# Performance work log

Hardware: AMD Instinct MI355X
Metric: run time of the kernel (lower is better)

The kernel has to match this reference:

```python
import jax, jax.numpy as jnp
import numpy as np

INPUT_CHANNELS = 64
OUT_CHANNELS = 64
OUT_DIM = 4
IN_FEAT = INPUT_CHANNELS * OUT_DIM * 2   # 512
OUT_FEAT = OUT_CHANNELS * OUT_DIM        # 256
BATCH = 65536


def setup_inputs() -> dict:
    key = jax.random.key(0)
    k_x, k_w, k_b = jax.random.split(key, 3)
    x = jax.random.normal(k_x, (BATCH, IN_FEAT), dtype=jnp.float32)
    weight = jax.random.normal(k_w, (OUT_FEAT, IN_FEAT), dtype=jnp.float32)
    bias = jax.random.normal(k_b, (1, OUT_FEAT), dtype=jnp.float32)
    return {"x": x, "weight": weight, "bias": bias}


def reference(x, weight, bias) -> jnp.ndarray:
    # Original: (x[:, None] * weight).sum(-1) / sqrt(input_channels) + 0.1*bias
    # Mathematically identical to a GEMM: x @ weight.T
    scale = 1.0 / jnp.sqrt(jnp.asarray(INPUT_CHANNELS, dtype=x.dtype))
    out = jnp.einsum('bi,oi->bo', x, weight) * scale  # [B, out_feat]
    out = out + bias * 0.1
    return out
```

## Files before the change

### kernel.cpp

```cpp
#include <hip/hip_runtime.h>
#include <hip/hip_bf16.h>


typedef __bf16 bf16;
typedef __attribute__((ext_vector_type(8))) __bf16 bf16x8;
typedef __attribute__((ext_vector_type(4))) __bf16 bf16x4;
typedef __attribute__((ext_vector_type(4))) float f32x4;

#define BATCH_ 65536
#define KDIM   512
#define NDIM   256
#define ROWS_PER_CHUNK   32
#define CHUNKS_PER_BLOCK 8
#define ROWS_PER_BLOCK   256
#define BN_BLOCK 128
#define BN_WAVE  16

__global__ __launch_bounds__(256) void wcvt_kernel(const float* __restrict__ w,
                                                   bf16* __restrict__ wb) {
    int i = (blockIdx.x * 256 + threadIdx.x) * 4;
    f32x4 v = *(const f32x4*)(w + i);
    bf16x4 o;
    o[0] = (bf16)(v.x * 0.125f);
    o[1] = (bf16)(v.y * 0.125f);
    o[2] = (bf16)(v.z * 0.125f);
    o[3] = (bf16)(v.w * 0.125f);
    *(bf16x4*)(wb + i) = o;
}

__global__ __launch_bounds__(512, 2) void gemm_kernel(const float* __restrict__ x,
                                                      const bf16* __restrict__ wb,
                                                      const float* __restrict__ bias,
                                                      float* __restrict__ out) {
    __shared__ __align__(16) char lds[2][32 * 1024];

    const int tid  = threadIdx.x;
    const int lane = tid & 63;
    const int w    = tid >> 6;
    const int q    = lane >> 4;
    const int l16  = lane & 15;

    const int  ng = blockIdx.x & 1;
    const long mg = blockIdx.x >> 1;
    const long row_base = mg * ROWS_PER_BLOCK;
    const int  n0 = ng * BN_BLOCK + w * BN_WAVE;

    bf16x8 wf[16];
#pragma unroll
    for (int kc = 0; kc < 16; ++kc)
        wf[kc] = *(const bf16x8*)(wb + (long)(n0 + l16) * KDIM + kc * 32 + q * 8);

    const float bv = 0.1f * bias[n0 + l16];

    const float* xw = x + (row_base + (long)w * 4) * KDIM + lane * 4;

    f32x4 ld[8];
#pragma unroll
    for (int j = 0; j < 4; ++j)
#pragma unroll
        for (int h = 0; h < 2; ++h)
            ld[j * 2 + h] = *(const f32x4*)(xw + (long)j * KDIM + h * 256);

    for (int t = 0; t < CHUNKS_PER_BLOCK; ++t) {
        char* buf = lds[t & 1];

#pragma unroll
        for (int j = 0; j < 4; ++j) {
            const int rr = w * 4 + j;
#pragma unroll
            for (int h = 0; h < 2; ++h) {
                f32x4 v = ld[j * 2 + h];
                bf16x4 o;
                o[0] = (bf16)v.x; o[1] = (bf16)v.y;
                o[2] = (bf16)v.z; o[3] = (bf16)v.w;
                const int g  = h * 32 + (lane >> 1);
                const int gs = g ^ (rr & 7);
                *(bf16x4*)(buf + rr * 1024 + gs * 16 + (lane & 1) * 8) = o;
            }
        }

        __syncthreads();

        if (t + 1 < CHUNKS_PER_BLOCK) {
#pragma unroll
            for (int j = 0; j < 4; ++j)
#pragma unroll
                for (int h = 0; h < 2; ++h)
                    ld[j * 2 + h] = *(const f32x4*)(xw + ((long)(t + 1) * 32 + j) * KDIM + h * 256);
        }

        f32x4 acc[2];
        acc[0] = (f32x4)0.0f;
        acc[1] = (f32x4)0.0f;
#pragma unroll
        for (int kc = 0; kc < 16; ++kc) {
#pragma unroll
            for (int mt = 0; mt < 2; ++mt) {
                const int rr = mt * 16 + l16;
                const int gs = (kc * 4 + q) ^ (rr & 7);
                bf16x8 a = *(const bf16x8*)(buf + rr * 1024 + gs * 16);
                acc[mt] = __builtin_amdgcn_mfma_f32_16x16x32_bf16(a, wf[kc], acc[mt], 0, 0, 0);
            }
        }

        const long row0 = row_base + (long)t * ROWS_PER_CHUNK;
#pragma unroll
        for (int mt = 0; mt < 2; ++mt)
#pragma unroll
            for (int r = 0; r < 4; ++r)
                out[(row0 + mt * 16 + q * 4 + r) * NDIM + n0 + l16] = acc[mt][r] + bv;
    }
}

extern "C" void kernel_launch(void* const* d_in, const int* in_sizes, int n_in,
                              void* d_out, int out_size, void* d_ws, size_t ws_size,
                              hipStream_t stream) {
    const float* x    = (const float*)d_in[0];
    const float* w    = (const float*)d_in[1];
    const float* bias = (const float*)d_in[2];
    float* out = (float*)d_out;
    bf16* wb   = (bf16*)d_ws;

    wcvt_kernel<<<(NDIM * KDIM) / (256 * 4), 256, 0, stream>>>(w, wb);
    gemm_kernel<<<(BATCH_ / ROWS_PER_BLOCK) * (NDIM / BN_BLOCK), 512, 0, stream>>>(x, wb, bias, out);
}
```

Before: 233.9 us.

## Compute full N per block and stage fp32 x directly into LDS

Each block now computes all 256 output columns instead of half, so every x row is read from global memory once rather than twice. x chunks are copied straight into LDS as fp32 using global_load_lds with double buffering, and the bf16 conversion moves to the LDS read just before the MFMA. The trade-offs are that each wave now keeps twice as many weight fragments in registers, which risks spills under the 512x2 launch bound. The unswizzled fp32 row-major LDS layout may also cause bank conflicts.

After: 230.9 us. No clear change (-1.3%).

```diff
diff --git a/kernel.cpp b/kernel.cpp
--- a/kernel.cpp
+++ b/kernel.cpp
@@ -10,11 +10,10 @@
 #define BATCH_ 65536
 #define KDIM   512
 #define NDIM   256
-#define ROWS_PER_CHUNK   32
-#define CHUNKS_PER_BLOCK 8
-#define ROWS_PER_BLOCK   256
-#define BN_BLOCK 128
-#define BN_WAVE  16
+#define CHUNK_ROWS 16
+#define CHUNKS 16
+#define ROWS_PER_BLOCK (CHUNK_ROWS * CHUNKS)
+#define CHUNK_BYTES (CHUNK_ROWS * KDIM * 4)
 
 __global__ __launch_bounds__(256) void wcvt_kernel(const float* __restrict__ w,
                                                    bf16* __restrict__ wb) {
@@ -28,87 +27,99 @@
     *(bf16x4*)(wb + i) = o;
 }
 
+__device__ __forceinline__ void stage_chunk(const float* xc, float* buf, int tid) {
+#pragma unroll
+    for (int p = 0; p < 4; ++p) {
+        const char* g = (const char*)xc + p * 8192 + tid * 16;
+        char* l = (char*)buf + p * 8192 + (tid >> 6) * 1024;
+        __builtin_amdgcn_global_load_lds(
+            (const __attribute__((address_space(1))) void*)g,
+            (__attribute__((address_space(3))) void*)l, 16, 0, 0);
+    }
+}
+
+__device__ __forceinline__ bf16x8 cvt_a(f32x4 lo, f32x4 hi) {
+    bf16x8 a;
+    a[0] = (bf16)lo.x; a[1] = (bf16)lo.y; a[2] = (bf16)lo.z; a[3] = (bf16)lo.w;
+    a[4] = (bf16)hi.x; a[5] = (bf16)hi.y; a[6] = (bf16)hi.z; a[7] = (bf16)hi.w;
+    return a;
+}
+
+__device__ __forceinline__ void compute_chunk(const float* buf,
+                                              const bf16x8 (&wf)[16][2],
+                                              int l16, int q, f32x4 (&acc)[2]) {
+    acc[0] = (f32x4)0.0f;
+    acc[1] = (f32x4)0.0f;
+    const float* rowp = buf + l16 * KDIM + q * 8;
+#pragma unroll
+    for (int kc = 0; kc < 16; ++kc) {
+        f32x4 lo = *(const f32x4*)(rowp + kc * 32);
+        f32x4 hi = *(const f32x4*)(rowp + kc * 32 + 4);
+        bf16x8 a = cvt_a(lo, hi);
+        acc[0] = __builtin_amdgcn_mfma_f32_16x16x32_bf16(a, wf[kc][0], acc[0], 0, 0, 0);
+        acc[1] = __builtin_amdgcn_mfma_f32_16x16x32_bf16(a, wf[kc][1], acc[1], 0, 0, 0);
+    }
+}
+
 __global__ __launch_bounds__(512, 2) void gemm_kernel(const float* __restrict__ x,
                                                       const bf16* __restrict__ wb,
                                                       const float* __restrict__ bias,
                                                       float* __restrict__ out) {
-    __shared__ __align__(16) char lds[2][32 * 1024];
+    __shared__ __align__(16) float bufA[CHUNK_ROWS * KDIM];
+    __shared__ __align__(16) float bufB[CHUNK_ROWS * KDIM];
 
     const int tid  = threadIdx.x;
     const int lane = tid & 63;
     const int w    = tid >> 6;
     const int q    = lane >> 4;
     const int l16  = lane & 15;
+    const int n0   = w * 32;
+    const long row_base = (long)blockIdx.x * ROWS_PER_BLOCK;
 
-    const int  ng = blockIdx.x & 1;
-    const long mg = blockIdx.x >> 1;
-    const long row_base = mg * ROWS_PER_BLOCK;
-    const int  n0 = ng * BN_BLOCK + w * BN_WAVE;
-
-    bf16x8 wf[16];
+    bf16x8 wf[16][2];
 #pragma unroll
     for (int kc = 0; kc < 16; ++kc)
-        wf[kc] = *(const bf16x8*)(wb + (long)(n0 + l16) * KDIM + kc * 32 + q * 8);
+#pragma unroll
+        for (int nt = 0; nt < 2; ++nt)
+            wf[kc][nt] = *(const bf16x8*)(wb + (long)(n0 + nt * 16 + l16) * KDIM
+                                             + kc * 32 + q * 8);
+    float bv[2];
+    bv[0] = 0.1f * bias[n0 + l16];
+    bv[1] = 0.1f * bias[n0 + 16 + l16];
 
-    const float bv = 0.1f * bias[n0 + l16];
+    const float* xblk = x + row_base * KDIM;
 
-    const float* xw = x + (row_base + (long)w * 4) * KDIM + lane * 4;
+    stage_chunk(xblk, bufA, tid);
+    __syncthreads();
 
-    f32x4 ld[8];
+    f32x4 acc[2];
+#pragma unroll 1
+    for (int t = 0; t < CHUNKS; t += 2) {
+        if (t + 1 < CHUNKS)
+            stage_chunk(xblk + (long)(t + 1) * CHUNK_ROWS * KDIM, bufB, tid);
+        compute_chunk(bufA, wf, l16, q, acc);
+        __syncthreads();
+        {
+            const long row0 = row_base + (long)t * CHUNK_ROWS;
 #pragma unroll
-    for (int j = 0; j < 4; ++j)
+            for (int nt = 0; nt < 2; ++nt)
 #pragma unroll
-        for (int h = 0; h < 2; ++h)
-            ld[j * 2 + h] = *(const f32x4*)(xw + (long)j * KDIM + h * 256);
-
-    for (int t = 0; t < CHUNKS_PER_BLOCK; ++t) {
-        char* buf = lds[t & 1];
-
-#pragma unroll
-        for (int j = 0; j < 4; ++j) {
-            const int rr = w * 4 + j;
-#pragma unroll
-            for (int h = 0; h < 2; ++h) {
-                f32x4 v = ld[j * 2 + h];
-                bf16x4 o;
-                o[0] = (bf16)v.x; o[1] = (bf16)v.y;
-                o[2] = (bf16)v.z; o[3] = (bf16)v.w;
-                const int g  = h * 32 + (lane >> 1);
-                const int gs = g ^ (rr & 7);
-                *(bf16x4*)(buf + rr * 1024 + gs * 16 + (lane & 1) * 8) = o;
-            }
+                for (int r = 0; r < 4; ++r)
+                    out[(row0 + q * 4 + r) * NDIM + n0 + nt * 16 + l16] = acc[nt][r] + bv[nt];
         }
 
+        if (t + 2 < CHUNKS)
+            stage_chunk(xblk + (long)(t + 2) * CHUNK_ROWS * KDIM, bufA, tid);
+        compute_chunk(bufB, wf, l16, q, acc);
         __syncthreads();
-
-        if (t + 1 < CHUNKS_PER_BLOCK) {
+        {
+            const long row0 = row_base + (long)(t + 1) * CHUNK_ROWS;
 #pragma unroll
-            for (int j = 0; j < 4; ++j)
+            for (int nt = 0; nt < 2; ++nt)
 #pragma unroll
-                for (int h = 0; h < 2; ++h)
-                    ld[j * 2 + h] = *(const f32x4*)(xw + ((long)(t + 1) * 32 + j) * KDIM + h * 256);
+                for (int r = 0; r < 4; ++r)
+                    out[(row0 + q * 4 + r) * NDIM + n0 + nt * 16 + l16] = acc[nt][r] + bv[nt];
         }
-
-        f32x4 acc[2];
-        acc[0] = (f32x4)0.0f;
-        acc[1] = (f32x4)0.0f;
-#pragma unroll
-        for (int kc = 0; kc < 16; ++kc) {
-#pragma unroll
-            for (int mt = 0; mt < 2; ++mt) {
-                const int rr = mt * 16 + l16;
-                const int gs = (kc * 4 + q) ^ (rr & 7);
-                bf16x8 a = *(const bf16x8*)(buf + rr * 1024 + gs * 16);
-                acc[mt] = __builtin_amdgcn_mfma_f32_16x16x32_bf16(a, wf[kc], acc[mt], 0, 0, 0);
-            }
-        }
-
-        const long row0 = row_base + (long)t * ROWS_PER_CHUNK;
-#pragma unroll
-        for (int mt = 0; mt < 2; ++mt)
-#pragma unroll
-            for (int r = 0; r < 4; ++r)
-                out[(row0 + mt * 16 + q * 4 + r) * NDIM + n0 + l16] = acc[mt][r] + bv;
     }
 }
 
@@ -122,5 +133,5 @@
     bf16* wb   = (bf16*)d_ws;
 
     wcvt_kernel<<<(NDIM * KDIM) / (256 * 4), 256, 0, stream>>>(w, wb);
-    gemm_kernel<<<(BATCH_ / ROWS_PER_BLOCK) * (NDIM / BN_BLOCK), 512, 0, stream>>>(x, wb, bias, out);
+    gemm_kernel<<<BATCH_ / ROWS_PER_BLOCK, 512, 0, stream>>>(x, wb, bias, out);
 }
```
